# Kernel tuning notes

Measured on AMD Instinct MI355X. Metric: run time of the kernel, lower is better.

The kernel has to match this reference:

```python
import jax, jax.numpy as jnp
import numpy as np

THRESH_POSITIVE_AFFINITY = 0.65
THRESH_POSITIVE_REGION = 0.6
LAMBDA_WEIGHT = 2.0
TOPK_FALLBACK = 500


def _single_image_loss(pre_loss, label, thresh_positive):
    """Vectorized version of the per-sample pos/neg split + hard-negative top-k.

    pre_loss, label: [B, N] (flattened per-sample masked MSE maps / GT maps).
    Returns scalar sum over the batch of (pos_loss + neg_loss) per sample.
    """
    B, N = pre_loss.shape
    pos_mask = label > thresh_positive                      # [B, N] bool
    n_pos = jnp.sum(pos_mask, axis=-1)                      # [B] int
    n_neg = N - n_pos                                       # [B] int

    # positive loss: mean over positive pixels (0 if none)
    pos_sum = jnp.sum(jnp.where(pos_mask, pre_loss, 0.0), axis=-1)
    pos_loss = jnp.where(n_pos > 0, pos_sum / jnp.maximum(n_pos, 1), 0.0)

    # negatives sorted descending; positives pushed to the end via -inf
    neg_vals = jnp.where(pos_mask, -jnp.inf, pre_loss)
    sorted_neg = -jnp.sort(-neg_vals, axis=-1)              # [B, N] descending
    sorted_neg = jnp.where(jnp.isfinite(sorted_neg), sorted_neg, 0.0)
    csum = jnp.cumsum(sorted_neg, axis=-1)                  # [B, N]

    # k = 3*n_pos if enough negatives, else all negatives (torch branch)
    k = jnp.minimum(3 * n_pos, n_neg)                       # [B]
    k_idx = jnp.maximum(k - 1, 0)
    topk_sum = jnp.take_along_axis(csum, k_idx[:, None], axis=-1)[:, 0]
    neg_loss = jnp.where(k > 0, topk_sum / jnp.maximum(k, 1), 0.0)

    # fallback when no positives: mean of global top-500 of the loss map
    top500 = jnp.mean(jax.lax.top_k(pre_loss, TOPK_FALLBACK)[0], axis=-1)

    per_sample = jnp.where(n_pos > 0, pos_loss + neg_loss, top500)
    return jnp.sum(per_sample)


def setup_inputs() -> dict:
    key = jax.random.key(0)
    k1, k2, k3, k4, k5 = jax.random.split(key, 5)
    shape = (32, 512, 512)
    return {
        "region_score_gt": jax.random.uniform(k1, shape, dtype=jnp.float32),
        "affinity_score_gt": jax.random.uniform(k2, shape, dtype=jnp.float32),
        "region_score_pred": jax.random.normal(k3, shape, dtype=jnp.float32),
        "affinity_score_pred": jax.random.normal(k4, shape, dtype=jnp.float32),
        "mask": jax.random.uniform(k5, shape, dtype=jnp.float32),
    }


def reference(region_score_gt, affinity_score_gt, region_score_pred,
              affinity_score_pred, mask):
    # clamp predictions to 1 where GT is positive and pred overshoots 1
    rp = jnp.where((region_score_gt > THRESH_POSITIVE_REGION)
                   & (region_score_pred > 1.0), 1.0, region_score_pred)
    ap = jnp.where((affinity_score_gt > THRESH_POSITIVE_AFFINITY)
                   & (affinity_score_pred > 1.0), 1.0, affinity_score_pred)

    loss_g = (rp - region_score_gt) ** 2 * mask             # masked MSE map
    loss_a = (ap - affinity_score_gt) ** 2 * mask

    B = loss_g.shape[0]
    char_loss = _single_image_loss(loss_g.reshape(B, -1),
                                   region_score_gt.reshape(B, -1),
                                   THRESH_POSITIVE_REGION)
    affi_loss = _single_image_loss(loss_a.reshape(B, -1),
                                   affinity_score_gt.reshape(B, -1),
                                   THRESH_POSITIVE_AFFINITY)
    return LAMBDA_WEIGHT * char_loss / B + affi_loss / B
```

## Files before the change

kernel.cpp:

```cpp
#include <hip/hip_runtime.h>


#define NPS (512 * 512)
#define BPS 32
#define EPB 8192
#define NB 32

constexpr float THR_REGION = 0.6f;
constexpr float THR_AFF    = 0.65f;

__global__ __launch_bounds__(256) void map_loss_pass1(
    const float* __restrict__ rg, const float* __restrict__ ag,
    const float* __restrict__ rp, const float* __restrict__ ap,
    const float* __restrict__ mk, float* __restrict__ part) {
  const int b   = blockIdx.y;
  const int tid = threadIdx.x;
  const size_t sbase = (size_t)b * NPS + (size_t)blockIdx.x * EPB;

  float v[6] = {0.f, 0.f, 0.f, 0.f, 0.f, 0.f};

#pragma unroll
  for (int jj = 0; jj < 8; ++jj) {
    const size_t base = sbase + (size_t)jj * 1024 + (size_t)tid * 4;
    const float4 g_r = *reinterpret_cast<const float4*>(rg + base);
    const float4 g_a = *reinterpret_cast<const float4*>(ag + base);
    const float4 p_r = *reinterpret_cast<const float4*>(rp + base);
    const float4 p_a = *reinterpret_cast<const float4*>(ap + base);
    const float4 m_4 = *reinterpret_cast<const float4*>(mk + base);
    const float* gr = reinterpret_cast<const float*>(&g_r);
    const float* ga = reinterpret_cast<const float*>(&g_a);
    const float* pr = reinterpret_cast<const float*>(&p_r);
    const float* pa = reinterpret_cast<const float*>(&p_a);
    const float* mm = reinterpret_cast<const float*>(&m_4);
#pragma unroll
    for (int j = 0; j < 4; ++j) {
      const float m = mm[j];
      {
        const float g = gr[j];
        float p = pr[j];
        const bool pos = g > THR_REGION;
        if (pos && p > 1.0f) p = 1.0f;
        const float d = p - g;
        const float l = d * d * m;
        if (pos) { v[0] += l; v[2] += 1.0f; } else { v[1] += l; }
      }
      {
        const float g = ga[j];
        float p = pa[j];
        const bool pos = g > THR_AFF;
        if (pos && p > 1.0f) p = 1.0f;
        const float d = p - g;
        const float l = d * d * m;
        if (pos) { v[3] += l; v[5] += 1.0f; } else { v[4] += l; }
      }
    }
  }

#pragma unroll
  for (int q = 0; q < 6; ++q)
#pragma unroll
    for (int off = 32; off > 0; off >>= 1)
      v[q] += __shfl_down(v[q], off, 64);

  __shared__ float sh[4][6];
  const int lane = tid & 63, wid = tid >> 6;
  if (lane == 0) {
#pragma unroll
    for (int q = 0; q < 6; ++q) sh[wid][q] = v[q];
  }
  __syncthreads();
  if (tid < 6) {
    const float s = sh[0][tid] + sh[1][tid] + sh[2][tid] + sh[3][tid];
    part[((size_t)b * BPS + blockIdx.x) * 6 + tid] = s;
  }
}

__device__ float topk_sum_row(const float* __restrict__ gt,
                              const float* __restrict__ pd,
                              const float* __restrict__ mm,
                              float thr, int k, bool negOnly) {
  unsigned prefix = 0;
  float sum_def = 0.f;
  int want = k;
  for (int shift = 24; shift >= 0; shift -= 8) {
    unsigned cnt[256];
    float bsum[256];
    for (int i = 0; i < 256; ++i) { cnt[i] = 0; bsum[i] = 0.f; }
    for (int j = 0; j < NPS; ++j) {
      const float g = gt[j];
      const bool pos = g > thr;
      if (negOnly && pos) continue;
      float p = pd[j];
      if (pos && p > 1.0f) p = 1.0f;
      const float d = p - g;
      const float vv = d * d * mm[j];
      const unsigned u = __float_as_uint(vv);
      if (shift < 24 && (u >> (shift + 8)) != (prefix >> (shift + 8))) continue;
      const unsigned bin = (u >> shift) & 255u;
      cnt[bin]++;
      bsum[bin] += vv;
    }
    int bin = 255;
    for (; bin > 0; --bin) {
      if ((int)cnt[bin] < want) { want -= (int)cnt[bin]; sum_def += bsum[bin]; }
      else break;
    }
    prefix |= ((unsigned)bin) << shift;
  }
  sum_def += (float)want * __uint_as_float(prefix);
  return sum_def;
}

__global__ __launch_bounds__(256) void map_loss_pass2(
    const float* __restrict__ part,
    const float* __restrict__ rg, const float* __restrict__ ag,
    const float* __restrict__ rp, const float* __restrict__ ap,
    const float* __restrict__ mk, float* __restrict__ out) {
  const int t = threadIdx.x;
  const int row = t >> 2;
  const int sub = t & 3;
  const int mapA = row >> 5;
  const int b = row & 31;

  float posSum = 0.f, negSum = 0.f, cntF = 0.f;
  for (int blk = sub; blk < BPS; blk += 4) {
    const float* p = part + ((size_t)b * BPS + blk) * 6 + mapA * 3;
    posSum += p[0];
    negSum += p[1];
    cntF   += p[2];
  }
#pragma unroll
  for (int msk = 1; msk <= 2; msk <<= 1) {
    posSum += __shfl_xor(posSum, msk, 64);
    negSum += __shfl_xor(negSum, msk, 64);
    cntF   += __shfl_xor(cntF, msk, 64);
  }

  __shared__ float sh[64];
  if (sub == 0) {
    const int npos = (int)cntF;
    const int nneg = NPS - npos;
    long long k = 3LL * npos;
    if (k > nneg) k = nneg;

    const float thr = mapA ? THR_AFF : THR_REGION;
    const float* gt = (mapA ? ag : rg) + (size_t)b * NPS;
    const float* pd = (mapA ? ap : rp) + (size_t)b * NPS;
    const float* mm = mk + (size_t)b * NPS;

    float per_sample;
    if (npos > 0) {
      const float pos_loss = posSum / (float)npos;
      float neg_loss = 0.f;
      if (k > 0) {
        if (k == (long long)nneg) {
          neg_loss = negSum / (float)nneg;
        } else {
          neg_loss = topk_sum_row(gt, pd, mm, thr, (int)k, true) / (float)k;
        }
      }
      per_sample = pos_loss + neg_loss;
    } else {
      per_sample = topk_sum_row(gt, pd, mm, thr, 500, false) / 500.0f;
    }
    sh[row] = per_sample;
  }
  __syncthreads();
  if (t == 0) {
    float char_sum = 0.f, affi_sum = 0.f;
    for (int i = 0; i < 32; ++i) { char_sum += sh[i]; affi_sum += sh[32 + i]; }
    out[0] = 2.0f * char_sum / (float)NB + affi_sum / (float)NB;
  }
}

extern "C" void kernel_launch(void* const* d_in, const int* in_sizes, int n_in,
                              void* d_out, int out_size, void* d_ws, size_t ws_size,
                              hipStream_t stream) {
  const float* rg = (const float*)d_in[0];
  const float* ag = (const float*)d_in[1];
  const float* rp = (const float*)d_in[2];
  const float* ap = (const float*)d_in[3];
  const float* mk = (const float*)d_in[4];
  float* out = (float*)d_out;
  float* part = (float*)d_ws;

  dim3 grid1(BPS, NB);
  map_loss_pass1<<<grid1, 256, 0, stream>>>(rg, ag, rp, ap, mk, part);
  map_loss_pass2<<<1, 256, 0, stream>>>(part, rg, ag, rp, ap, mk, out);
}
```

Measured before the change: 32.99 us.

## Double pass1 block count and hoist all loads before compute

Halves the elements per block in the streaming reduction (64 blocks per sample instead of 32) and issues all twenty float4 loads per thread before any arithmetic. The aim is more memory-level parallelism and more resident waves to better saturate HBM bandwidth. It costs more registers per thread and twice as many partial results for the second pass to reduce.

```diff
diff --git a/kernel.cpp b/kernel.cpp
--- a/kernel.cpp
+++ b/kernel.cpp
@@ -2,8 +2,8 @@
 
 
 #define NPS (512 * 512)
-#define BPS 32
-#define EPB 8192
+#define BPS 64
+#define EPB 4096
 #define NB 32
 
 constexpr float THR_REGION = 0.6f;
@@ -15,23 +15,32 @@
     const float* __restrict__ mk, float* __restrict__ part) {
   const int b   = blockIdx.y;
   const int tid = threadIdx.x;
-  const size_t sbase = (size_t)b * NPS + (size_t)blockIdx.x * EPB;
+  const size_t sbase = (size_t)b * NPS + (size_t)blockIdx.x * EPB + (size_t)tid * 4;
+
+  const float4* Gr = reinterpret_cast<const float4*>(rg + sbase);
+  const float4* Ga = reinterpret_cast<const float4*>(ag + sbase);
+  const float4* Pr = reinterpret_cast<const float4*>(rp + sbase);
+  const float4* Pa = reinterpret_cast<const float4*>(ap + sbase);
+  const float4* Mm = reinterpret_cast<const float4*>(mk + sbase);
+
+  float4 vg[4], va[4], vp[4], vq[4], vm[4];
+#pragma unroll
+  for (int jj = 0; jj < 4; ++jj) {
+    vg[jj] = Gr[jj * 256];
+    va[jj] = Ga[jj * 256];
+    vp[jj] = Pr[jj * 256];
+    vq[jj] = Pa[jj * 256];
+    vm[jj] = Mm[jj * 256];
+  }
 
   float v[6] = {0.f, 0.f, 0.f, 0.f, 0.f, 0.f};
-
 #pragma unroll
-  for (int jj = 0; jj < 8; ++jj) {
-    const size_t base = sbase + (size_t)jj * 1024 + (size_t)tid * 4;
-    const float4 g_r = *reinterpret_cast<const float4*>(rg + base);
-    const float4 g_a = *reinterpret_cast<const float4*>(ag + base);
-    const float4 p_r = *reinterpret_cast<const float4*>(rp + base);
-    const float4 p_a = *reinterpret_cast<const float4*>(ap + base);
-    const float4 m_4 = *reinterpret_cast<const float4*>(mk + base);
-    const float* gr = reinterpret_cast<const float*>(&g_r);
-    const float* ga = reinterpret_cast<const float*>(&g_a);
-    const float* pr = reinterpret_cast<const float*>(&p_r);
-    const float* pa = reinterpret_cast<const float*>(&p_a);
-    const float* mm = reinterpret_cast<const float*>(&m_4);
+  for (int jj = 0; jj < 4; ++jj) {
+    const float* gr = reinterpret_cast<const float*>(&vg[jj]);
+    const float* ga = reinterpret_cast<const float*>(&va[jj]);
+    const float* pr = reinterpret_cast<const float*>(&vp[jj]);
+    const float* pa = reinterpret_cast<const float*>(&vq[jj]);
+    const float* mm = reinterpret_cast<const float*>(&vm[jj]);
 #pragma unroll
     for (int j = 0; j < 4; ++j) {
       const float m = mm[j];
```

Result: slower. 35.31 us (+7.0%).
